# Performance work log

Measured on AMD Instinct MI355X. Metric: run time of the kernel, lower is better.

The kernel has to match this reference:

```python
import jax, jax.numpy as jnp
import numpy as np

FEATURE_DIM = 2048
EMBED_DIM = 512
HIDDEN_DIM = 512
VOCAB_SIZE = 10000
ATT_DIM = 512
BATCH = 32
NUM_PIXELS = 196
MAX_LEN = 20


def setup_inputs() -> dict:
    key = jax.random.key(0)
    ks = jax.random.split(key, 16)
    def p(k, shape, scale=0.02):
        return jax.random.normal(k, shape, dtype=jnp.float32) * scale
    return {
        "features": jax.random.normal(ks[0], (BATCH, NUM_PIXELS, FEATURE_DIM), dtype=jnp.float32),
        "captions": jax.random.randint(ks[1], (BATCH, MAX_LEN), 0, VOCAB_SIZE),
        "emb": p(ks[2], (VOCAB_SIZE, EMBED_DIM)),
        "W_ih": p(ks[3], (4 * HIDDEN_DIM, EMBED_DIM + FEATURE_DIM)),
        "b_ih": jnp.zeros((4 * HIDDEN_DIM,), dtype=jnp.float32),
        "W_hh": p(ks[4], (4 * HIDDEN_DIM, HIDDEN_DIM)),
        "b_hh": jnp.zeros((4 * HIDDEN_DIM,), dtype=jnp.float32),
        "fc_W": p(ks[5], (VOCAB_SIZE, HIDDEN_DIM)),
        "fc_b": jnp.zeros((VOCAB_SIZE,), dtype=jnp.float32),
        "enc_W": p(ks[6], (ATT_DIM, FEATURE_DIM)),
        "enc_b": jnp.zeros((ATT_DIM,), dtype=jnp.float32),
        "dec_W": p(ks[7], (ATT_DIM, HIDDEN_DIM)),
        "dec_b": jnp.zeros((ATT_DIM,), dtype=jnp.float32),
        "full_W": p(ks[8], (1, ATT_DIM)),
        "full_b": jnp.zeros((1,), dtype=jnp.float32),
    }


def reference(features, captions, emb, W_ih, b_ih, W_hh, b_hh, fc_W, fc_b,
              enc_W, enc_b, dec_W, dec_b, full_W, full_b):
    # embeddings: [B, T, E] -> scan over time as [T, B, E]
    embeddings = emb[captions]
    xs = jnp.swapaxes(embeddings, 0, 1)
    B = features.shape[0]
    h0 = jnp.zeros((B, HIDDEN_DIM), dtype=features.dtype)
    c0 = jnp.zeros((B, HIDDEN_DIM), dtype=features.dtype)
    # encoder projection of features is time-invariant: [B, P, A]
    enc_proj = jnp.einsum('bpf,af->bpa', features, enc_W) + enc_b

    def step(carry, x_t):
        h, c = carry
        # Bahdanau attention
        dec_proj = h @ dec_W.T + dec_b                      # [B, A]
        e = jnp.einsum('bpa,a->bp', jax.nn.relu(enc_proj + dec_proj[:, None, :]), full_W[0]) + full_b[0]
        alpha = jax.nn.softmax(e, axis=1)                   # [B, P]
        context = jnp.einsum('bp,bpf->bf', alpha, features) # [B, F]
        # LSTMCell
        lstm_in = jnp.concatenate([x_t, context], axis=1)
        gates = lstm_in @ W_ih.T + b_ih + h @ W_hh.T + b_hh
        i, f, g, o = jnp.split(gates, 4, axis=1)
        i = jax.nn.sigmoid(i)
        f = jax.nn.sigmoid(f)
        g = jnp.tanh(g)
        o = jax.nn.sigmoid(o)
        c_new = f * c + i * g
        h_new = o * jnp.tanh(c_new)
        # dropout in eval mode = identity
        out = h_new @ fc_W.T + fc_b                         # [B, V]
        return (h_new, c_new), out

    _, outs = jax.lax.scan(step, (h0, c0), xs)
    return jnp.swapaxes(outs, 0, 1)  # [B, T, V]
```

## Files before the change

kernel.cpp:

```cpp
#include <hip/hip_runtime.h>
#include <math.h>

#define B_   32
#define P_   196
#define F_   2048
#define E_   512
#define H_   512
#define V_   10000
#define T_   20
#define GSZ  8
#define NBLK (B_ * GSZ)

typedef unsigned short ushort_t;
typedef ushort_t u16x8 __attribute__((ext_vector_type(8)));
typedef ushort_t u16x2 __attribute__((ext_vector_type(2)));
typedef short    bf16x8 __attribute__((ext_vector_type(8)));
typedef float    f32x4  __attribute__((ext_vector_type(4)));

__device__ __forceinline__ ushort_t bf_rne(float x) {
    union { float f; unsigned u; } v; v.f = x;
    unsigned r = v.u + 0x7FFFu + ((v.u >> 16) & 1u);
    return (ushort_t)(r >> 16);
}
__device__ __forceinline__ float b2f(ushort_t u) {
    union { unsigned u; float f; } v; v.u = ((unsigned)u) << 16;
    return v.f;
}

__device__ __forceinline__ void gl_lds16(const ushort_t* g, ushort_t* l) {
    __builtin_amdgcn_global_load_lds(
        (const __attribute__((address_space(1))) void*)g,
        (__attribute__((address_space(3))) void*)l, 16, 0, 0);
}

__device__ __forceinline__ int permc(int chunk) {
    int gi = chunk >> 6, r = chunk & 63;
    return (r & 7) * 32 + (r >> 3) * 4 + gi;
}

__global__ __launch_bounds__(256)
void cvt_all_kernel(const float* __restrict__ feat, const float* __restrict__ enc_W,
                    const float* __restrict__ fc_W, const float* __restrict__ dec_W,
                    const float* __restrict__ W_ih, const float* __restrict__ W_hh,
                    const float* __restrict__ emb, const int* __restrict__ captions,
                    const float* __restrict__ b_ih, const float* __restrict__ b_hh,
                    ushort_t* __restrict__ featB, ushort_t* __restrict__ encWB,
                    ushort_t* __restrict__ fcWB, ushort_t* __restrict__ decWB,
                    ushort_t* __restrict__ WihCB, ushort_t* __restrict__ WihEB,
                    ushort_t* __restrict__ WhhT, ushort_t* __restrict__ XB,
                    float* __restrict__ bsum, float* __restrict__ zbuf)
{
    const int blk = blockIdx.x, tid = threadIdx.x;
    if (blk < 6272) {
        size_t i = (size_t)blk * 2048 + tid * 8;
        float4 a = *(const float4*)&feat[i], b = *(const float4*)&feat[i + 4];
        u16x8 o; o[0]=bf_rne(a.x); o[1]=bf_rne(a.y); o[2]=bf_rne(a.z); o[3]=bf_rne(a.w);
        o[4]=bf_rne(b.x); o[5]=bf_rne(b.y); o[6]=bf_rne(b.z); o[7]=bf_rne(b.w);
        *(u16x8*)&featB[i] = o;
    } else if (blk < 6784) {
        size_t i = (size_t)(blk - 6272) * 2048 + tid * 8;
        float4 a = *(const float4*)&enc_W[i], b = *(const float4*)&enc_W[i + 4];
        u16x8 o; o[0]=bf_rne(a.x); o[1]=bf_rne(a.y); o[2]=bf_rne(a.z); o[3]=bf_rne(a.w);
        o[4]=bf_rne(b.x); o[5]=bf_rne(b.y); o[6]=bf_rne(b.z); o[7]=bf_rne(b.w);
        *(u16x8*)&encWB[i] = o;
    } else if (blk < 9284) {
        size_t i = (size_t)(blk - 6784) * 2048 + tid * 8;
        float4 a = *(const float4*)&fc_W[i], b = *(const float4*)&fc_W[i + 4];
        u16x8 o; o[0]=bf_rne(a.x); o[1]=bf_rne(a.y); o[2]=bf_rne(a.z); o[3]=bf_rne(a.w);
        o[4]=bf_rne(b.x); o[5]=bf_rne(b.y); o[6]=bf_rne(b.z); o[7]=bf_rne(b.w);
        *(u16x8*)&fcWB[i] = o;
    } else if (blk < 9412) {
        size_t i = (size_t)(blk - 9284) * 2048 + tid * 8;
        float4 a = *(const float4*)&dec_W[i], b = *(const float4*)&dec_W[i + 4];
        u16x8 o; o[0]=bf_rne(a.x); o[1]=bf_rne(a.y); o[2]=bf_rne(a.z); o[3]=bf_rne(a.w);
        o[4]=bf_rne(b.x); o[5]=bf_rne(b.y); o[6]=bf_rne(b.z); o[7]=bf_rne(b.w);
        *(u16x8*)&decWB[i] = o;
    } else if (blk < 11460) {
        int j = blk - 9412, f = tid * 8;
        int Pj = permc(j >> 3) * 8 + (j & 7);
        const float* s = &W_ih[(size_t)j * 2560 + 512 + f];
        float4 a = *(const float4*)&s[0], b = *(const float4*)&s[4];
        u16x8 o; o[0]=bf_rne(a.x); o[1]=bf_rne(a.y); o[2]=bf_rne(a.z); o[3]=bf_rne(a.w);
        o[4]=bf_rne(b.x); o[5]=bf_rne(b.y); o[6]=bf_rne(b.z); o[7]=bf_rne(b.w);
        *(u16x8*)&WihCB[(size_t)Pj * 2048 + f] = o;
    } else if (blk < 11972) {
        size_t idx = (size_t)(blk - 11460) * 2048 + tid * 8;
        int j = (int)(idx >> 9), f = (int)(idx & 511);
        int Pj = permc(j >> 3) * 8 + (j & 7);
        const float* s = &W_ih[(size_t)j * 2560 + f];
        float4 a = *(const float4*)&s[0], b = *(const float4*)&s[4];
        u16x8 o; o[0]=bf_rne(a.x); o[1]=bf_rne(a.y); o[2]=bf_rne(a.z); o[3]=bf_rne(a.w);
        o[4]=bf_rne(b.x); o[5]=bf_rne(b.y); o[6]=bf_rne(b.z); o[7]=bf_rne(b.w);
        *(u16x8*)&WihEB[(size_t)Pj * 512 + f] = o;
    } else if (blk < 12484) {
        int k = blk - 11972, j0 = tid * 8;
        int nc = permc(tid);
        u16x8 o;
#pragma unroll
        for (int q = 0; q < 8; q++) o[q] = bf_rne(W_hh[(size_t)(j0 + q) * 512 + k]);
        *(u16x8*)&WhhT[(size_t)k * 2048 + nc * 8] = o;
    } else if (blk < 13124) {
        int m = blk - 12484;
        int tt = m >> 5, b = m & 31;
        int cap = captions[b * T_ + tt];
        int i = tid * 2;
        u16x2 o;
        o[0] = bf_rne(emb[(size_t)cap * 512 + i]);
        o[1] = bf_rne(emb[(size_t)cap * 512 + i + 1]);
        *(u16x2*)&XB[(size_t)m * 512 + i] = o;
    } else {
        int nc = permc(tid);
        int j0 = tid * 8;
#pragma unroll
        for (int q = 0; q < 8; q++) {
            bsum[nc * 8 + q] = b_ih[j0 + q] + b_hh[j0 + q];
            zbuf[j0 + q] = 0.f;
        }
    }
}

__global__ __launch_bounds__(256)
void mfma_gemm_kernel(const ushort_t* __restrict__ A, const ushort_t* __restrict__ B,
                      const float* __restrict__ bias, ushort_t* __restrict__ Cb,
                      float* __restrict__ Cf, int K, int N, int mode)
{
    __shared__ ushort_t As[128][32];
    __shared__ ushort_t Bs[128][32];
    const int tid = threadIdx.x;
    const int m0 = blockIdx.x * 128, n0 = blockIdx.y * 128;
    const int wave = tid >> 6, lane = tid & 63;
    const int wm = (wave & 1) * 64, wn = (wave >> 1) * 64;
    const int lm = lane & 15, lk = (lane >> 4) * 8;

    f32x4 acc[4][4];
#pragma unroll
    for (int mt = 0; mt < 4; mt++)
#pragma unroll
        for (int nt = 0; nt < 4; nt++)
#pragma unroll
            for (int r = 0; r < 4; r++) acc[mt][nt][r] = 0.f;

    for (int k0 = 0; k0 < K; k0 += 32) {
#pragma unroll
        for (int i = 0; i < 2; i++) {
            int gi  = tid + i * 256;
            int row = gi >> 2;
            int gr  = (gi & 3) * 8;
            ushort_t* lbA = &As[0][0] + (size_t)(wave * 64 + i * 256) * 8;
            ushort_t* lbB = &Bs[0][0] + (size_t)(wave * 64 + i * 256) * 8;
            gl_lds16(&A[(size_t)(m0 + row) * K + k0 + gr], lbA);
            int brow = n0 + row; if (brow >= N) brow = N - 1;
            gl_lds16(&B[(size_t)brow * K + k0 + gr], lbB);
        }
        __syncthreads();
        bf16x8 af[4], bv[4];
#pragma unroll
        for (int mt = 0; mt < 4; mt++)
            af[mt] = *(const bf16x8*)&As[wm + mt * 16 + lm][lk];
#pragma unroll
        for (int nt = 0; nt < 4; nt++)
            bv[nt] = *(const bf16x8*)&Bs[wn + nt * 16 + lm][lk];
#pragma unroll
        for (int mt = 0; mt < 4; mt++)
#pragma unroll
            for (int nt = 0; nt < 4; nt++)
                acc[mt][nt] = __builtin_amdgcn_mfma_f32_16x16x32_bf16(
                    af[mt], bv[nt], acc[mt][nt], 0, 0, 0);
        __syncthreads();
    }

    const int rb = (lane >> 4) * 4;
#pragma unroll
    for (int nt = 0; nt < 4; nt++) {
        int n = n0 + wn + nt * 16 + lm;
        int nc = n < N ? n : N - 1;
        float bz = (mode == 3) ? 0.f : bias[nc];
#pragma unroll
        for (int mt = 0; mt < 4; mt++) {
            int mbase = m0 + wm + mt * 16 + rb;
#pragma unroll
            for (int r = 0; r < 4; r++) {
                int m = mbase + r;
                float v = acc[mt][nt][r] + ((mode == 3) ? bias[m] : bz);
                if (mode == 0 || mode == 3) {
                    Cb[(size_t)m * N + n] = bf_rne(v);
                } else if (n < N) {
                    int crow = (mode == 1) ? ((m & 31) * 20 + (m >> 5)) : m;
                    Cf[(size_t)crow * N + n] = v;
                }
            }
        }
    }
}

__device__ __forceinline__ void wait_cnt(unsigned* p, unsigned target) {
    if (threadIdx.x == 0) {
        while (__hip_atomic_load(p, __ATOMIC_RELAXED, __HIP_MEMORY_SCOPE_AGENT) < target)
            __builtin_amdgcn_s_sleep(1);
    }
    __syncthreads();
}

__global__ __launch_bounds__(256, 1)
void persist_kernel(float* __restrict__ hbuf,
                    ushort_t* __restrict__ hseqB,
                    const ushort_t* __restrict__ encPT,
                    const ushort_t* __restrict__ decWB,
                    const float* __restrict__ dec_b,
                    const float* __restrict__ full_W,
                    const float* __restrict__ full_b,
                    const ushort_t* __restrict__ GB,
                    const ushort_t* __restrict__ WhhT,
                    const float* __restrict__ xproj,
                    float* __restrict__ epartG,
                    unsigned* __restrict__ hcnt,
                    unsigned* __restrict__ ecnt)
{
    __shared__ ushort_t Gs[196][256];
    __shared__ ushort_t ePs[64][200];
    __shared__ float hsh[512];
    __shared__ float fws[512];
    __shared__ float dps64[64];
    __shared__ float es[200];
    __shared__ float al[200];
    __shared__ float sred[8][32][9];
    __shared__ float gsh[256];

    const int tid = threadIdx.x;
    const int b = blockIdx.x & 31;
    const int s = blockIdx.x >> 5;
    unsigned* hcn = &hcnt[b * 32];
    unsigned* ecn = &ecnt[b * 32];
    float* epb = epartG + (size_t)b * 1600;

    {
        const int r0 = tid >> 5, c = (tid & 31) * 8;
        for (int i = 0; i < 25; i++) {
            int r = i * 8 + r0;
            if (r < 196)
                *(u16x8*)&Gs[r][c] =
                    *(const u16x8*)&GB[((size_t)(b * P_ + r)) * 2048 + s * 256 + c];
        }
    }
    for (int it = 0; it < 25; it++) {
        int idx = it * 256 + tid;
        if (idx < 6272) {
            int a = idx / 98, pp = idx - a * 98;
            *(u16x2*)&ePs[a][pp * 2] =
                *(const u16x2*)&encPT[(size_t)(s * 64 + a) * 6272 + b * P_ + pp * 2];
        }
    }
    if (tid < 128)
        *(float4*)&fws[tid * 4] = *(const float4*)&full_W[tid * 4];

    const int lane = tid & 63, wave = tid >> 6;
    const int g16 = lane >> 4, gl = lane & 15;
    const int kg = tid >> 5, cg = tid & 31;
    const float fb0 = full_b[0];
    float c_reg = 0.f;

    u16x8 dreg[16];
#pragma unroll
    for (int q = 0; q < 4; q++) {
        int a = wave * 16 + q * 4 + g16;
        const ushort_t* wr = decWB + (size_t)(s * 64 + a) * 512;
#pragma unroll
        for (int jj = 0; jj < 4; jj++)
            dreg[q * 4 + jj] = *(const u16x8*)&wr[jj * 128 + gl * 8];
    }

    for (int t = 0; t < T_; t++) {
        float gx = xproj[(size_t)(t * 32 + b) * 2048 + s * 256 + tid];

        if (t == 0) {
            hsh[tid * 2] = 0.f; hsh[tid * 2 + 1] = 0.f;
        } else {
            wait_cnt(hcn, 8u * (unsigned)t);
            const float* hb = hbuf + ((size_t)(t & 1) * 32 + b) * 512;
            hsh[tid * 2] = __hip_atomic_load(&hb[tid * 2],
                                             __ATOMIC_RELAXED, __HIP_MEMORY_SCOPE_AGENT);
            hsh[tid * 2 + 1] = __hip_atomic_load(&hb[tid * 2 + 1],
                                             __ATOMIC_RELAXED, __HIP_MEMORY_SCOPE_AGENT);
        }
        __syncthreads();

        if (t == 0) {
            if (tid < 64) dps64[tid] = dec_b[s * 64 + tid];
        } else {
#pragma unroll
            for (int q = 0; q < 4; q++) {
                int a = wave * 16 + q * 4 + g16;
                float sacc = 0.f;
#pragma unroll
                for (int jj = 0; jj < 4; jj++) {
                    u16x8 wv = dreg[q * 4 + jj];
                    float4 h0 = *(float4*)&hsh[jj * 128 + gl * 8];
                    float4 h1 = *(float4*)&hsh[jj * 128 + gl * 8 + 4];
                    sacc += b2f(wv[0]) * h0.x + b2f(wv[1]) * h0.y
                          + b2f(wv[2]) * h0.z + b2f(wv[3]) * h0.w
                          + b2f(wv[4]) * h1.x + b2f(wv[5]) * h1.y
                          + b2f(wv[6]) * h1.z + b2f(wv[7]) * h1.w;
                }
                sacc += __shfl_xor(sacc, 1, 64); sacc += __shfl_xor(sacc, 2, 64);
                sacc += __shfl_xor(sacc, 4, 64); sacc += __shfl_xor(sacc, 8, 64);
                if (gl == 0) dps64[a] = sacc + dec_b[s * 64 + a];
            }
        }
        __syncthreads();

        if (tid < 196) {
            float e = 0.f;
#pragma unroll 8
            for (int a = 0; a < 64; a++)
                e += fmaxf(b2f(ePs[a][tid]) + dps64[a], 0.f) * fws[s * 64 + a];
            __hip_atomic_store(&epb[s * 200 + tid], e,
                               __ATOMIC_RELAXED, __HIP_MEMORY_SCOPE_AGENT);
        }
        __syncthreads();
        if (tid == 0)
            __hip_atomic_fetch_add(ecn, 1u,
                                   __ATOMIC_RELEASE, __HIP_MEMORY_SCOPE_AGENT);

        {
            float wa[8] = {0.f,0.f,0.f,0.f,0.f,0.f,0.f,0.f};
            const ushort_t* wp = WhhT + (size_t)(kg * 64) * 2048 + s * 256 + cg * 8;
#pragma unroll 8
            for (int kk = 0; kk < 64; kk++) {
                u16x8 wv = *(const u16x8*)&wp[(size_t)kk * 2048];
                float hv = hsh[kg * 64 + kk];
#pragma unroll
                for (int q = 0; q < 8; q++) wa[q] += b2f(wv[q]) * hv;
            }
#pragma unroll
            for (int q = 0; q < 8; q++) sred[kg][cg][q] = wa[q];
        }
        __syncthreads();
        float g = gx;
#pragma unroll
        for (int k2 = 0; k2 < 8; k2++) g += sred[k2][tid >> 3][tid & 7];

        wait_cnt(ecn, 8u * (unsigned)(t + 1));
        if (tid < 196) {
            float e = fb0;
#pragma unroll
            for (int s2 = 0; s2 < 8; s2++)
                e += __hip_atomic_load(&epb[s2 * 200 + tid],
                                       __ATOMIC_RELAXED, __HIP_MEMORY_SCOPE_AGENT);
            es[tid] = e;
        }
        __syncthreads();
        if (tid < 64) {
            float v[4]; int pv[4]; int n = 0;
            for (int q = 0; q < 4; q++) {
                int p = tid + 64 * q;
                if (p < P_) { pv[n] = p; v[n] = es[p]; n++; }
            }
            float m = -1e30f;
            for (int q = 0; q < n; q++) m = fmaxf(m, v[q]);
#pragma unroll
            for (int off = 32; off > 0; off >>= 1) m = fmaxf(m, __shfl_xor(m, off, 64));
            float ssum = 0.f;
            for (int q = 0; q < n; q++) { v[q] = expf(v[q] - m); ssum += v[q]; }
#pragma unroll
            for (int off = 32; off > 0; off >>= 1) ssum += __shfl_xor(ssum, off, 64);
            float rinv = 1.f / ssum;
            for (int q = 0; q < n; q++) al[pv[q]] = v[q] * rinv;
        }
        __syncthreads();

        {
            int p0 = (kg < 4) ? kg * 25 : 100 + (kg - 4) * 24;
            int np = (kg < 4) ? 25 : 24;
            float pa[8] = {0.f,0.f,0.f,0.f,0.f,0.f,0.f,0.f};
#pragma unroll 4
            for (int i = 0; i < np; i++) {
                int p = p0 + i;
                float av = al[p];
                u16x8 gv = *(const u16x8*)&Gs[p][cg * 8];
#pragma unroll
                for (int q = 0; q < 8; q++) pa[q] += b2f(gv[q]) * av;
            }
#pragma unroll
            for (int q = 0; q < 8; q++) sred[kg][cg][q] = pa[q];
        }
        __syncthreads();
#pragma unroll
        for (int k2 = 0; k2 < 8; k2++) g += sred[k2][tid >> 3][tid & 7];
        gsh[tid] = g;
        __syncthreads();

        if (tid < 64) {
            int ri = tid >> 3, e = tid & 7;
            float gi = gsh[ri * 32 + e];
            float gf = gsh[ri * 32 + 8 + e];
            float gg = gsh[ri * 32 + 16 + e];
            float go = gsh[ri * 32 + 24 + e];
            float ig = 1.f / (1.f + expf(-gi));
            float fg = 1.f / (1.f + expf(-gf));
            float g_ = tanhf(gg);
            float og = 1.f / (1.f + expf(-go));
            c_reg = fg * c_reg + ig * g_;
            float hn = og * tanhf(c_reg);
            int u = 8 * s + 64 * ri + e;
            float* ho = hbuf + ((size_t)((t + 1) & 1) * 32 + b) * 512 + u;
            __hip_atomic_store(ho, hn, __ATOMIC_RELAXED, __HIP_MEMORY_SCOPE_AGENT);
            hseqB[(size_t)(t + 1) * 16384 + b * 512 + u] = bf_rne(hn);
        }
        __syncthreads();
        if (tid == 0)
            __hip_atomic_fetch_add(hcn, 1u,
                                   __ATOMIC_RELEASE, __HIP_MEMORY_SCOPE_AGENT);
    }
}

extern "C" void kernel_launch(void* const* d_in, const int* in_sizes, int n_in,
                              void* d_out, int out_size, void* d_ws, size_t ws_size,
                              hipStream_t stream)
{
    (void)in_sizes; (void)n_in; (void)out_size; (void)ws_size;
    const float* feat   = (const float*)d_in[0];
    const int*   caps   = (const int*)  d_in[1];
    const float* emb    = (const float*)d_in[2];
    const float* W_ih   = (const float*)d_in[3];
    const float* b_ih   = (const float*)d_in[4];
    const float* W_hh   = (const float*)d_in[5];
    const float* b_hh   = (const float*)d_in[6];
    const float* fc_W   = (const float*)d_in[7];
    const float* fc_b   = (const float*)d_in[8];
    const float* enc_W  = (const float*)d_in[9];
    const float* enc_b  = (const float*)d_in[10];
    const float* dec_W  = (const float*)d_in[11];
    const float* dec_b  = (const float*)d_in[12];
    const float* full_W = (const float*)d_in[13];
    const float* full_b = (const float*)d_in[14];
    float* out = (float*)d_out;

    char* w = (char*)d_ws;
    ushort_t* featB = (ushort_t*)w;              w += 25690112;
    ushort_t* encWB = (ushort_t*)w;              w += 2097152;
    ushort_t* fcWB  = (ushort_t*)w;              w += 10240000;
    ushort_t* decWB = (ushort_t*)w;              w += 524288;
    ushort_t* WihCB = (ushort_t*)w;              w += 8388608;
    ushort_t* WihEB = (ushort_t*)w;              w += 2097152;
    ushort_t* WhhT  = (ushort_t*)w;              w += 2097152;
    ushort_t* XB    = (ushort_t*)w;              w += 655360;
    ushort_t* encPT = (ushort_t*)w;              w += 6422528;
    ushort_t* GB    = (ushort_t*)w;              w += 25690112;
    float*    xproj = (float*)w;                 w += 5242880;
    float*    bsum  = (float*)w;                 w += 8192;
    float*    zbuf  = (float*)w;                 w += 8192;
    float*    hbuf  = (float*)w;                 w += 131072;
    ushort_t* hseqB = (ushort_t*)w;              w += 688128;
    unsigned* hcnt  = (unsigned*)w;              w += 4096;
    unsigned* ecnt  = (unsigned*)w;              w += 4096;
    float*    epartG= (float*)w;                 w += 204800;

    hipMemsetAsync(hcnt, 0, 8192, stream);

    cvt_all_kernel<<<13125, 256, 0, stream>>>(
        feat, enc_W, fc_W, dec_W, W_ih, W_hh, emb, caps, b_ih, b_hh,
        featB, encWB, fcWB, decWB, WihCB, WihEB, WhhT, XB, bsum, zbuf);

    mfma_gemm_kernel<<<dim3(4, 49), 256, 0, stream>>>(
        encWB, featB, enc_b, encPT, nullptr, 2048, 6272, 3);

    mfma_gemm_kernel<<<dim3(49, 16), 256, 0, stream>>>(
        featB, WihCB, zbuf, GB, nullptr, 2048, 2048, 0);

    mfma_gemm_kernel<<<dim3(5, 16), 256, 0, stream>>>(
        XB, WihEB, bsum, nullptr, xproj, 512, 2048, 2);

    persist_kernel<<<NBLK, 256, 0, stream>>>(
        hbuf, hseqB, encPT, decWB, dec_b, full_W, full_b,
        GB, WhhT, xproj, epartG, hcnt, ecnt);

    mfma_gemm_kernel<<<dim3(5, 79), 256, 0, stream>>>(
        hseqB + 16384, fcWB, fc_b, nullptr, out, 512, V_, 1);
}
```

Before: 840.5 us.

## Replace counter barriers with tag-stamped 64-bit data words in persistent LSTM

The inter-block handoff of hidden state and attention partial scores now packs the step number into the high 32 bits of each 64-bit value. Consumers spin on the data words directly, so the separate counter atomics, the release fetch-adds and the extra block-wide barriers go away. This cuts per-step synchronisation latency in the 20-step recurrence. The cost is doubled storage and traffic for the exchanged values, plus per-thread polling by many lanes instead of a single thread. The decoder bias is also cached in shared memory.

```diff
diff --git a/kernel.cpp b/kernel.cpp
--- a/kernel.cpp
+++ b/kernel.cpp
@@ -12,6 +12,7 @@
 #define NBLK (B_ * GSZ)
 
 typedef unsigned short ushort_t;
+typedef unsigned long long u64_t;
 typedef ushort_t u16x8 __attribute__((ext_vector_type(8)));
 typedef ushort_t u16x2 __attribute__((ext_vector_type(2)));
 typedef short    bf16x8 __attribute__((ext_vector_type(8)));
@@ -25,6 +26,12 @@
 __device__ __forceinline__ float b2f(ushort_t u) {
     union { unsigned u; float f; } v; v.u = ((unsigned)u) << 16;
     return v.f;
+}
+__device__ __forceinline__ unsigned f2u(float f) {
+    union { float f; unsigned u; } v; v.f = f; return v.u;
+}
+__device__ __forceinline__ float u2f(unsigned u) {
+    union { unsigned u; float f; } v; v.u = u; return v.f;
 }
 
 __device__ __forceinline__ void gl_lds16(const ushort_t* g, ushort_t* l) {
@@ -193,16 +200,8 @@
     }
 }
 
-__device__ __forceinline__ void wait_cnt(unsigned* p, unsigned target) {
-    if (threadIdx.x == 0) {
-        while (__hip_atomic_load(p, __ATOMIC_RELAXED, __HIP_MEMORY_SCOPE_AGENT) < target)
-            __builtin_amdgcn_s_sleep(1);
-    }
-    __syncthreads();
-}
-
 __global__ __launch_bounds__(256, 1)
-void persist_kernel(float* __restrict__ hbuf,
+void persist_kernel(u64_t* __restrict__ hbufQ,
                     ushort_t* __restrict__ hseqB,
                     const ushort_t* __restrict__ encPT,
                     const ushort_t* __restrict__ decWB,
@@ -212,15 +211,14 @@
                     const ushort_t* __restrict__ GB,
                     const ushort_t* __restrict__ WhhT,
                     const float* __restrict__ xproj,
-                    float* __restrict__ epartG,
-                    unsigned* __restrict__ hcnt,
-                    unsigned* __restrict__ ecnt)
+                    u64_t* __restrict__ epartQ)
 {
     __shared__ ushort_t Gs[196][256];
     __shared__ ushort_t ePs[64][200];
     __shared__ float hsh[512];
     __shared__ float fws[512];
     __shared__ float dps64[64];
+    __shared__ float dbias[64];
     __shared__ float es[200];
     __shared__ float al[200];
     __shared__ float sred[8][32][9];
@@ -229,9 +227,8 @@
     const int tid = threadIdx.x;
     const int b = blockIdx.x & 31;
     const int s = blockIdx.x >> 5;
-    unsigned* hcn = &hcnt[b * 32];
-    unsigned* ecn = &ecnt[b * 32];
-    float* epb = epartG + (size_t)b * 1600;
+    u64_t* hbq = hbufQ + (size_t)b * 512;
+    u64_t* epq = epartQ + (size_t)b * 1600;
 
     {
         const int r0 = tid >> 5, c = (tid & 31) * 8;
@@ -252,6 +249,8 @@
     }
     if (tid < 128)
         *(float4*)&fws[tid * 4] = *(const float4*)&full_W[tid * 4];
+    if (tid < 64)
+        dbias[tid] = dec_b[s * 64 + tid];
 
     const int lane = tid & 63, wave = tid >> 6;
     const int g16 = lane >> 4, gl = lane & 15;
@@ -275,17 +274,25 @@
         if (t == 0) {
             hsh[tid * 2] = 0.f; hsh[tid * 2 + 1] = 0.f;
         } else {
-            wait_cnt(hcn, 8u * (unsigned)t);
-            const float* hb = hbuf + ((size_t)(t & 1) * 32 + b) * 512;
-            hsh[tid * 2] = __hip_atomic_load(&hb[tid * 2],
-                                             __ATOMIC_RELAXED, __HIP_MEMORY_SCOPE_AGENT);
-            hsh[tid * 2 + 1] = __hip_atomic_load(&hb[tid * 2 + 1],
-                                             __ATOMIC_RELAXED, __HIP_MEMORY_SCOPE_AGENT);
+            const unsigned tag = (unsigned)t;
+            u64_t w0 = 0, w1 = 0;
+            bool g0 = false, g1 = false;
+            while (!(g0 && g1)) {
+                if (!g0) w0 = __hip_atomic_load(&hbq[tid * 2],
+                                __ATOMIC_RELAXED, __HIP_MEMORY_SCOPE_AGENT);
+                if (!g1) w1 = __hip_atomic_load(&hbq[tid * 2 + 1],
+                                __ATOMIC_RELAXED, __HIP_MEMORY_SCOPE_AGENT);
+                g0 = g0 || ((unsigned)(w0 >> 32) == tag);
+                g1 = g1 || ((unsigned)(w1 >> 32) == tag);
+                if (!(g0 && g1)) __builtin_amdgcn_s_sleep(1);
+            }
+            hsh[tid * 2]     = u2f((unsigned)w0);
+            hsh[tid * 2 + 1] = u2f((unsigned)w1);
         }
         __syncthreads();
 
         if (t == 0) {
-            if (tid < 64) dps64[tid] = dec_b[s * 64 + tid];
+            if (tid < 64) dps64[tid] = dbias[tid];
         } else {
 #pragma unroll
             for (int q = 0; q < 4; q++) {
@@ -303,7 +310,7 @@
                 }
                 sacc += __shfl_xor(sacc, 1, 64); sacc += __shfl_xor(sacc, 2, 64);
                 sacc += __shfl_xor(sacc, 4, 64); sacc += __shfl_xor(sacc, 8, 64);
-                if (gl == 0) dps64[a] = sacc + dec_b[s * 64 + a];
+                if (gl == 0) dps64[a] = sacc + dbias[a];
             }
         }
         __syncthreads();
@@ -313,13 +320,10 @@
 #pragma unroll 8
             for (int a = 0; a < 64; a++)
                 e += fmaxf(b2f(ePs[a][tid]) + dps64[a], 0.f) * fws[s * 64 + a];
-            __hip_atomic_store(&epb[s * 200 + tid], e,
+            u64_t w = ((u64_t)(unsigned)(t + 1) << 32) | (u64_t)f2u(e);
+            __hip_atomic_store(&epq[s * 200 + tid], w,
                                __ATOMIC_RELAXED, __HIP_MEMORY_SCOPE_AGENT);
         }
-        __syncthreads();
-        if (tid == 0)
-            __hip_atomic_fetch_add(ecn, 1u,
-                                   __ATOMIC_RELEASE, __HIP_MEMORY_SCOPE_AGENT);
 
         {
             float wa[8] = {0.f,0.f,0.f,0.f,0.f,0.f,0.f,0.f};
@@ -339,13 +343,25 @@
 #pragma unroll
         for (int k2 = 0; k2 < 8; k2++) g += sred[k2][tid >> 3][tid & 7];
 
-        wait_cnt(ecn, 8u * (unsigned)(t + 1));
         if (tid < 196) {
+            const unsigned tag = (unsigned)(t + 1);
+            u64_t wv[8];
+            unsigned ok = 0;
+            while (ok != 0xffu) {
+#pragma unroll
+                for (int s2 = 0; s2 < 8; s2++)
+                    if (!(ok & (1u << s2)))
+                        wv[s2] = __hip_atomic_load(&epq[s2 * 200 + tid],
+                                     __ATOMIC_RELAXED, __HIP_MEMORY_SCOPE_AGENT);
+#pragma unroll
+                for (int s2 = 0; s2 < 8; s2++)
+                    if (!(ok & (1u << s2)) && ((unsigned)(wv[s2] >> 32) == tag))
+                        ok |= 1u << s2;
+                if (ok != 0xffu) __builtin_amdgcn_s_sleep(1);
+            }
             float e = fb0;
 #pragma unroll
-            for (int s2 = 0; s2 < 8; s2++)
-                e += __hip_atomic_load(&epb[s2 * 200 + tid],
-                                       __ATOMIC_RELAXED, __HIP_MEMORY_SCOPE_AGENT);
+            for (int s2 = 0; s2 < 8; s2++) e += u2f((unsigned)wv[s2]);
             es[tid] = e;
         }
         __syncthreads();
@@ -402,14 +418,12 @@
             c_reg = fg * c_reg + ig * g_;
             float hn = og * tanhf(c_reg);
             int u = 8 * s + 64 * ri + e;
-            float* ho = hbuf + ((size_t)((t + 1) & 1) * 32 + b) * 512 + u;
-            __hip_atomic_store(ho, hn, __ATOMIC_RELAXED, __HIP_MEMORY_SCOPE_AGENT);
+            u64_t w = ((u64_t)(unsigned)(t + 1) << 32) | (u64_t)f2u(hn);
+            __hip_atomic_store(&hbq[u], w,
+                               __ATOMIC_RELAXED, __HIP_MEMORY_SCOPE_AGENT);
             hseqB[(size_t)(t + 1) * 16384 + b * 512 + u] = bf_rne(hn);
         }
         __syncthreads();
-        if (tid == 0)
-            __hip_atomic_fetch_add(hcn, 1u,
-                                   __ATOMIC_RELEASE, __HIP_MEMORY_SCOPE_AGENT);
     }
 }
 
@@ -449,13 +463,11 @@
     float*    xproj = (float*)w;                 w += 5242880;
     float*    bsum  = (float*)w;                 w += 8192;
     float*    zbuf  = (float*)w;                 w += 8192;
-    float*    hbuf  = (float*)w;                 w += 131072;
     ushort_t* hseqB = (ushort_t*)w;              w += 688128;
-    unsigned* hcnt  = (unsigned*)w;              w += 4096;
-    unsigned* ecnt  = (unsigned*)w;              w += 4096;
-    float*    epartG= (float*)w;                 w += 204800;
-
-    hipMemsetAsync(hcnt, 0, 8192, stream);
+    u64_t*    hbufQ = (u64_t*)w;                 w += 131072;
+    u64_t*    epartQ= (u64_t*)w;                 w += 409600;
+
+    hipMemsetAsync(hbufQ, 0, 131072 + 409600, stream);
 
     cvt_all_kernel<<<13125, 256, 0, stream>>>(
         feat, enc_W, fc_W, dec_W, W_ih, W_hh, emb, caps, b_ih, b_hh,
@@ -471,8 +483,8 @@
         XB, WihEB, bsum, nullptr, xproj, 512, 2048, 2);
 
     persist_kernel<<<NBLK, 256, 0, stream>>>(
-        hbuf, hseqB, encPT, decWB, dec_b, full_W, full_b,
-        GB, WhhT, xproj, epartG, hcnt, ecnt);
+        hbufQ, hseqB, encPT, decWB, dec_b, full_W, full_b,
+        GB, WhhT, xproj, epartQ);
 
     mfma_gemm_kernel<<<dim3(5, 79), 256, 0, stream>>>(
         hseqB + 16384, fcWB, fc_b, nullptr, out, 512, V_, 1);
```

Result: faster. 733.7 us (-12.7%).
